# Performance work log

Hardware: AMD Instinct MI355X
Metric: run time of the kernel (lower is better)

The kernel has to match this reference:

```python
import jax, jax.numpy as jnp
import numpy as np

N, FIN, FOUT = 4096, 512, 256
ALPHA = 0.2          # LeakyReLU negative slope
NEG_INF = -9e15      # mask value from the torch source


def setup_inputs() -> dict:
    key = jax.random.key(0)
    ks = jax.random.split(key, 11)
    h = jax.random.normal(ks[0], (N, FIN), dtype=jnp.float32)
    adj_n = jax.random.randint(ks[1], (N, N), 0, 2, dtype=jnp.int32)
    adj_d = jax.random.randint(ks[2], (N, N), 0, 2, dtype=jnp.int32)
    G_nd = jax.random.normal(ks[3], (2, N, FOUT), dtype=jnp.float32)
    # learned parameters (xavier-ish scale)
    W_n = jax.random.normal(ks[4], (FIN, FOUT), dtype=jnp.float32) * 0.05
    a1_n = jax.random.normal(ks[5], (FOUT, 1), dtype=jnp.float32) * 0.05
    a2_n = jax.random.normal(ks[6], (FOUT, 1), dtype=jnp.float32) * 0.05
    W_d = jax.random.normal(ks[7], (FIN, FOUT), dtype=jnp.float32) * 0.05
    a1_d = jax.random.normal(ks[8], (FOUT, 1), dtype=jnp.float32) * 0.05
    a2_d = jax.random.normal(ks[9], (FOUT, 1), dtype=jnp.float32) * 0.05
    scale = jnp.zeros((1,), dtype=jnp.float32)
    return {"h": h, "adj_n": adj_n, "adj_d": adj_d, "G_nd": G_nd,
            "W_n": W_n, "a1_n": a1_n, "a2_n": a2_n,
            "W_d": W_d, "a1_d": a1_d, "a2_d": a2_d, "scale": scale}


def _gat(h, adj, W, a1, a2):
    # Wh: [N, FOUT]
    Wh = h @ W
    # outer-sum attention logits: e[i,j] = leakyrelu(Wh_i.a1 + Wh_j.a2)
    e = jax.nn.leaky_relu((Wh @ a1) + (Wh @ a2).T, negative_slope=ALPHA)  # [N, N]
    att = jnp.where(adj > 0, e, jnp.float32(NEG_INF))
    att = jax.nn.softmax(att, axis=-1)
    # dropout is identity in eval mode
    return jax.nn.elu(att @ Wh)  # [N, FOUT]


def reference(h, adj_n, adj_d, G_nd, W_n, a1_n, a2_n, W_d, a1_d, a2_d, scale):
    f_n_S = _gat(h, adj_n, W_n, a1_n, a2_n)
    f_d_S = _gat(h, adj_d, W_d, a1_d, a2_d)
    # The G_nd cross-attention branch (f_nd_C) in the torch source is computed
    # but never used in the returned value; omitted here (jit would DCE it).
    return f_n_S + f_d_S
```

## Files before the change

### kernel.cpp

```cpp
#include <hip/hip_runtime.h>

#define N_NODES 4096
#define FIN     512
#define FOUT    256
#define NSPLIT  4
#define NTILES  ((N_NODES / NSPLIT) / 64)

typedef __attribute__((ext_vector_type(8))) short bf16x8s;
typedef __attribute__((ext_vector_type(4))) float f32x4;
typedef __attribute__((ext_vector_type(8))) unsigned short u16x8;
typedef unsigned short u16;
typedef unsigned int   u32;
typedef unsigned long long u64;

__device__ inline u16 f2b(float f) {
    union { float f; unsigned int u; } v; v.f = f;
    unsigned int r = v.u + 0x7fffu + ((v.u >> 16) & 1u);
    return (u16)(r >> 16);
}

__global__ __launch_bounds__(256) void prep_kernel(
    const float* __restrict__ h, const float* __restrict__ Wn,
    const float* __restrict__ Wd,
    const int* __restrict__ adjn, const int* __restrict__ adjd,
    u16* __restrict__ hb, u16* __restrict__ WTb, u16* __restrict__ bits16,
    float* __restrict__ s12)
{
    __shared__ u16 tl[64 * 72];
    const int t = threadIdx.x;
    const int bid = blockIdx.x;

    if (bid < 1024) {
        int idx = (bid * 256 + t) * 8;
        float4 f0 = *(const float4*)&h[idx];
        float4 f1 = *(const float4*)&h[idx + 4];
        u16x8 o;
        o[0]=f2b(f0.x); o[1]=f2b(f0.y); o[2]=f2b(f0.z); o[3]=f2b(f0.w);
        o[4]=f2b(f1.x); o[5]=f2b(f1.y); o[6]=f2b(f1.z); o[7]=f2b(f1.w);
        *(u16x8*)&hb[idx] = o;
    } else if (bid < 3072) {
        const int lane = t & 63, w = t >> 6;
        const long gw = (long)(bid - 1024) * 4 + w;
        const long base = gw * 4096;
        const int* p = (base < (1L << 24)) ? (adjn + base)
                                           : (adjd + (base - (1L << 24)));
        const int4* src = (const int4*)p + lane * 4;
        u16* dst = bits16 + (base >> 4) + lane;
        #pragma unroll
        for (int s = 0; s < 4; ++s) {
            int4 a = src[s * 256 + 0];
            int4 b = src[s * 256 + 1];
            int4 c = src[s * 256 + 2];
            int4 d = src[s * 256 + 3];
            u32 m = 0;
            m |= (u32)(a.x > 0) << 0;  m |= (u32)(a.y > 0) << 1;
            m |= (u32)(a.z > 0) << 2;  m |= (u32)(a.w > 0) << 3;
            m |= (u32)(b.x > 0) << 4;  m |= (u32)(b.y > 0) << 5;
            m |= (u32)(b.z > 0) << 6;  m |= (u32)(b.w > 0) << 7;
            m |= (u32)(c.x > 0) << 8;  m |= (u32)(c.y > 0) << 9;
            m |= (u32)(c.z > 0) << 10; m |= (u32)(c.w > 0) << 11;
            m |= (u32)(d.x > 0) << 12; m |= (u32)(d.y > 0) << 13;
            m |= (u32)(d.z > 0) << 14; m |= (u32)(d.w > 0) << 15;
            dst[s * 64] = (u16)m;
        }
    } else if (bid < 3136) {
        int id = bid - 3072;
        int kx = id & 7, ny = (id >> 3) & 3, b = id >> 5;
        const float* W = b ? Wd : Wn;
        int k0 = kx * 64, n0 = ny * 64;
        int kr = t >> 2, nc0 = (t & 3) * 16;
        const float* src = W + (size_t)(k0 + kr) * FOUT + n0 + nc0;
        #pragma unroll
        for (int jv = 0; jv < 4; ++jv) {
            float4 f = *(const float4*)(src + jv * 4);
            tl[(nc0 + jv * 4 + 0) * 72 + kr] = f2b(f.x);
            tl[(nc0 + jv * 4 + 1) * 72 + kr] = f2b(f.y);
            tl[(nc0 + jv * 4 + 2) * 72 + kr] = f2b(f.z);
            tl[(nc0 + jv * 4 + 3) * 72 + kr] = f2b(f.w);
        }
        __syncthreads();
        int n = t >> 2, kc0 = (t & 3) * 16;
        u16* dst = WTb + ((size_t)b << 17) + (size_t)(n0 + n) * FIN + k0 + kc0;
        *(uint4*)dst       = *(uint4*)&tl[n * 72 + kc0];
        *(uint4*)(dst + 8) = *(uint4*)&tl[n * 72 + kc0 + 8];
    } else {
        float4 z = {0.f, 0.f, 0.f, 0.f};
        float4* p4 = (float4*)s12;
        #pragma unroll
        for (int k = 0; k < 16; ++k) p4[k * 256 + t] = z;
    }
}

__global__ __launch_bounds__(256) void wh_gemm_kernel(
    const u16* __restrict__ hb, const u16* __restrict__ WTb,
    const float* __restrict__ a1n, const float* __restrict__ a2n,
    const float* __restrict__ a1d, const float* __restrict__ a2d,
    u16* __restrict__ WhT, float* __restrict__ s1, float* __restrict__ s2)
{
    __shared__ u16 smem[8192];
    u16* a_lds = smem;
    u16* b_lds = smem + 4096;

    const int t = threadIdx.x, lane = t & 63, w = t >> 6;
    const int q = lane >> 4, ln = lane & 15;
    const int i0 = blockIdx.x * 64, n0 = blockIdx.y * 64, b = blockIdx.z;
    const u16* wt = WTb + ((size_t)b << 17);

    f32x4 acc[4];
    #pragma unroll
    for (int i = 0; i < 4; ++i) acc[i] = (f32x4){0.f, 0.f, 0.f, 0.f};

    for (int kt = 0; kt < 8; ++kt) {
        const int k0 = kt * 64;
        __syncthreads();
        #pragma unroll
        for (int it = 0; it < 2; ++it) {
            int chunk = it * 256 + t;
            int r = chunk >> 3, kc = chunk & 7;
            const u16* g = hb + (size_t)(i0 + r) * FIN + k0 + ((kc ^ (r & 7)) * 8);
            u16* l = a_lds + (it * 256 + w * 64) * 8;
            __builtin_amdgcn_global_load_lds(
                (const __attribute__((address_space(1))) void*)g,
                (__attribute__((address_space(3))) void*)l, 16, 0, 0);
        }
        #pragma unroll
        for (int it = 0; it < 2; ++it) {
            int chunk = it * 256 + t;
            int n = chunk >> 3, kc = chunk & 7;
            const u16* g = wt + (size_t)(n0 + n) * FIN + k0 + ((kc ^ (n & 7)) * 8);
            u16* l = b_lds + (it * 256 + w * 64) * 8;
            __builtin_amdgcn_global_load_lds(
                (const __attribute__((address_space(1))) void*)g,
                (__attribute__((address_space(3))) void*)l, 16, 0, 0);
        }
        __syncthreads();
        #pragma unroll
        for (int ks = 0; ks < 2; ++ks) {
            int sw = ((ks * 4 + q) ^ (ln & 7)) * 8;
            bf16x8s af = *(const bf16x8s*)&a_lds[(w * 16 + ln) * 64 + sw];
            #pragma unroll
            for (int nt = 0; nt < 4; ++nt) {
                bf16x8s bfv = *(const bf16x8s*)&b_lds[(nt * 16 + ln) * 64 + sw];
                acc[nt] = __builtin_amdgcn_mfma_f32_16x16x32_bf16(af, bfv, acc[nt], 0, 0, 0);
            }
        }
    }

    {
        const float* a1 = b ? a1d : a1n;
        const float* a2 = b ? a2d : a2n;
        float s1p[4] = {0.f, 0.f, 0.f, 0.f};
        float s2p[4] = {0.f, 0.f, 0.f, 0.f};
        #pragma unroll
        for (int nt = 0; nt < 4; ++nt) {
            float va1 = a1[n0 + nt * 16 + ln];
            float va2 = a2[n0 + nt * 16 + ln];
            #pragma unroll
            for (int r = 0; r < 4; ++r) {
                s1p[r] += acc[nt][r] * va1;
                s2p[r] += acc[nt][r] * va2;
            }
        }
        #pragma unroll
        for (int r = 0; r < 4; ++r) {
            #pragma unroll
            for (int off = 8; off >= 1; off >>= 1) {
                s1p[r] += __shfl_xor(s1p[r], off);
                s2p[r] += __shfl_xor(s2p[r], off);
            }
            if (ln == 0) {
                int row = i0 + w * 16 + q * 4 + r;
                atomicAdd(&s1[b * N_NODES + row], s1p[r]);
                atomicAdd(&s2[b * N_NODES + row], s2p[r]);
            }
        }
    }

    __syncthreads();
    #pragma unroll
    for (int nt = 0; nt < 4; ++nt)
        #pragma unroll
        for (int r = 0; r < 4; ++r)
            smem[(nt * 16 + ln) * 72 + (w * 16 + q * 4 + r)] = f2b(acc[nt][r]);
    __syncthreads();
    {
        const int nl = t >> 2, is = (t & 3) * 16;
        u16* dst = WhT + ((size_t)b << 20) + (size_t)(n0 + nl) * N_NODES + i0 + is;
        *(uint4*)dst       = *(uint4*)&smem[nl * 72 + is];
        *(uint4*)(dst + 8) = *(uint4*)&smem[nl * 72 + is + 8];
    }
}

__global__ __launch_bounds__(256) void attn_kernel(
    const u32* __restrict__ bits,
    const u16* __restrict__ WhT,
    const float* __restrict__ s1, const float* __restrict__ s2,
    float* __restrict__ num_ws, float* __restrict__ den_ws)
{
    __shared__ u16 wht_lds[256 * 64];
    __shared__ u16 p_lds[64 * 64];
    __shared__ float den_lds[64];

    const int t = threadIdx.x, lane = t & 63, w = t >> 6;
    const int q = lane >> 4, ln = lane & 15;
    const int b = blockIdx.z, split = blockIdx.y;
    const int i0 = blockIdx.x * 64;

    const u16* whtB = WhT + ((size_t)b << 20);
    const float* s1b = s1 + b * N_NODES;
    const float* s2b = s2 + b * N_NODES;

    const int pr = t >> 3;
    const int cw = t & 7;
    const int pc = cw * 8;
    const int bsh = (cw & 3) * 8;
    const float s1v0 = s1b[i0 + pr];
    const float s1v1 = s1b[i0 + pr + 32];
    const u32* bitrow0 = bits + (size_t)b * (N_NODES * (N_NODES / 32))
                              + (size_t)(i0 + pr) * (N_NODES / 32) + (cw >> 2);
    const u32* bitrow1 = bitrow0 + 32 * (N_NODES / 32);

    if (t < 64) den_lds[t] = 0.f;

    f32x4 acc[4][4];
    #pragma unroll
    for (int mt = 0; mt < 4; ++mt)
        #pragma unroll
        for (int nt = 0; nt < 4; ++nt) acc[mt][nt] = (f32x4){0.f, 0.f, 0.f, 0.f};

    const int jbase = split * (N_NODES / NSPLIT);
    u32 bw0_pf = bitrow0[jbase >> 5];
    u32 bw1_pf = bitrow1[jbase >> 5];
    float4 sv0_pf = *(const float4*)&s2b[jbase + pc];
    float4 sv1_pf = *(const float4*)&s2b[jbase + pc + 4];

    for (int jt = 0; jt < NTILES; ++jt) {
        const int j0 = jbase + jt * 64;
        __syncthreads();
        #pragma unroll
        for (int it = 0; it < 8; ++it) {
            int chunk = it * 256 + t;
            int n = chunk >> 3, kc = chunk & 7;
            const u16* g = whtB + (size_t)n * N_NODES + j0 + ((kc ^ (n & 7)) * 8);
            u16* l = wht_lds + (it * 256 + w * 64) * 8;
            __builtin_amdgcn_global_load_lds(
                (const __attribute__((address_space(1))) void*)g,
                (__attribute__((address_space(3))) void*)l, 16, 0, 0);
        }
        u32 bw0 = bw0_pf, bw1 = bw1_pf;
        float4 sv0 = sv0_pf, sv1 = sv1_pf;
        if (jt < NTILES - 1) {
            bw0_pf = bitrow0[(j0 + 64) >> 5];
            bw1_pf = bitrow1[(j0 + 64) >> 5];
            sv0_pf = *(const float4*)&s2b[j0 + 64 + pc];
            sv1_pf = *(const float4*)&s2b[j0 + 64 + pc + 4];
        }
        u32 m0 = (bw0 >> bsh) & 0xffu;
        u32 m1 = (bw1 >> bsh) & 0xffu;
        float svf[8] = {sv0.x, sv0.y, sv0.z, sv0.w, sv1.x, sv1.y, sv1.z, sv1.w};
        float d0 = 0.f, d1 = 0.f;
        u16x8 pk0, pk1;
        #pragma unroll
        for (int jj = 0; jj < 8; ++jj) {
            float sv = svf[jj];
            float x0 = s1v0 + sv, x1 = s1v1 + sv;
            float p0 = ((m0 >> jj) & 1u) ? __expf(fmaxf(x0, 0.2f * x0)) : 0.f;
            float p1 = ((m1 >> jj) & 1u) ? __expf(fmaxf(x1, 0.2f * x1)) : 0.f;
            d0 += p0; d1 += p1;
            pk0[jj] = f2b(p0); pk1[jj] = f2b(p1);
        }
        d0 += __shfl_down(d0, 4, 8); d1 += __shfl_down(d1, 4, 8);
        d0 += __shfl_down(d0, 2, 8); d1 += __shfl_down(d1, 2, 8);
        d0 += __shfl_down(d0, 1, 8); d1 += __shfl_down(d1, 1, 8);
        if ((t & 7) == 0) { den_lds[pr] += d0; den_lds[pr + 32] += d1; }
        int swp = ((cw ^ (pr & 7)) * 8);
        *(u16x8*)&p_lds[pr * 64 + swp] = pk0;
        *(u16x8*)&p_lds[(pr + 32) * 64 + swp] = pk1;
        __syncthreads();
        #pragma unroll
        for (int ks = 0; ks < 2; ++ks) {
            int sw = ((ks * 4 + q) ^ (ln & 7)) * 8;
            bf16x8s af[4];
            #pragma unroll
            for (int mt = 0; mt < 4; ++mt)
                af[mt] = *(const bf16x8s*)&p_lds[(mt * 16 + ln) * 64 + sw];
            #pragma unroll
            for (int nt = 0; nt < 4; ++nt) {
                bf16x8s bfv = *(const bf16x8s*)&wht_lds[(w * 64 + nt * 16 + ln) * 64 + sw];
                #pragma unroll
                for (int mt = 0; mt < 4; ++mt)
                    acc[mt][nt] = __builtin_amdgcn_mfma_f32_16x16x32_bf16(af[mt], bfv, acc[mt][nt], 0, 0, 0);
            }
        }
    }
    const size_t pbase = (size_t)(b * NSPLIT + split) * N_NODES;
    #pragma unroll
    for (int mt = 0; mt < 4; ++mt)
        #pragma unroll
        for (int r = 0; r < 4; ++r) {
            int row = mt * 16 + q * 4 + r;
            #pragma unroll
            for (int nt = 0; nt < 4; ++nt)
                num_ws[(pbase + i0 + row) * FOUT + w * 64 + nt * 16 + ln] = acc[mt][nt][r];
        }
    if (t < 64) den_ws[pbase + i0 + t] = den_lds[t];
}

__global__ __launch_bounds__(256) void reduce_kernel(
    const float* __restrict__ num_ws, const float* __restrict__ den_ws,
    float* __restrict__ out)
{
    int gid = blockIdx.x * 256 + threadIdx.x;
    int i = gid >> 6;
    int f4 = (gid & 63) * 4;
    float4 o = {0.f, 0.f, 0.f, 0.f};
    #pragma unroll
    for (int b = 0; b < 2; ++b) {
        float4 num = {0.f, 0.f, 0.f, 0.f};
        float den = 0.f;
        #pragma unroll
        for (int s = 0; s < NSPLIT; ++s) {
            const float4 v = *(const float4*)&num_ws[((size_t)(b * NSPLIT + s) * N_NODES + i) * FOUT + f4];
            num.x += v.x; num.y += v.y; num.z += v.z; num.w += v.w;
            den += den_ws[(size_t)(b * NSPLIT + s) * N_NODES + i];
        }
        float inv = 1.0f / den;
        float e0 = num.x * inv, e1 = num.y * inv, e2 = num.z * inv, e3 = num.w * inv;
        o.x += (e0 > 0.f) ? e0 : expm1f(e0);
        o.y += (e1 > 0.f) ? e1 : expm1f(e1);
        o.z += (e2 > 0.f) ? e2 : expm1f(e2);
        o.w += (e3 > 0.f) ? e3 : expm1f(e3);
    }
    *(float4*)&out[(size_t)i * FOUT + f4] = o;
}

extern "C" void kernel_launch(void* const* d_in, const int* in_sizes, int n_in,
                              void* d_out, int out_size, void* d_ws, size_t ws_size,
                              hipStream_t stream) {
    const float* h    = (const float*)d_in[0];
    const int*   adjn = (const int*)d_in[1];
    const int*   adjd = (const int*)d_in[2];
    const float* Wn   = (const float*)d_in[4];
    const float* a1n  = (const float*)d_in[5];
    const float* a2n  = (const float*)d_in[6];
    const float* Wd   = (const float*)d_in[7];
    const float* a1d  = (const float*)d_in[8];
    const float* a2d  = (const float*)d_in[9];

    char* ws = (char*)d_ws;
    u16*  WhT  = (u16*)ws;
    u16*  bits = (u16*)(ws + ((size_t)4 << 20));
    float* s1  = (float*)(ws + ((size_t)8 << 20));
    float* s2  = s1 + 2 * N_NODES;
    float* den = s2 + 2 * N_NODES;
    u16*  hb   = (u16*)(ws + ((size_t)8 << 20) + ((size_t)256 << 10));
    u16*  WTb  = (u16*)(ws + ((size_t)12 << 20) + ((size_t)256 << 10));
    float* num = (float*)(ws + ((size_t)8 << 20) + ((size_t)256 << 10));

    prep_kernel<<<3137, 256, 0, stream>>>(h, Wn, Wd, adjn, adjd, hb, WTb, bits, s1);
    wh_gemm_kernel<<<dim3(64, 4, 2), 256, 0, stream>>>(hb, WTb, a1n, a2n, a1d, a2d, WhT, s1, s2);
    attn_kernel<<<dim3(64, NSPLIT, 2), 256, 0, stream>>>((const u32*)bits, WhT, s1, s2, num, den);
    reduce_kernel<<<1024, 256, 0, stream>>>(num, den, (float*)d_out);
}
```

Baseline: 221.5 us.

## Read int adjacency directly in attention kernel instead of prepacking bitmasks

Removes the prep stage that packed both 4096x4096 int32 adjacency matrices into bitmasks, and has the attention kernel load int4 adjacency values directly with prefetch. This avoids one full read of the adjacency plus a bitmask write and reread across kernels. The attention kernel now streams 32x more mask bytes per tile (128 MB total), so it may become bandwidth-bound where it was not before.

```diff
diff --git a/kernel.cpp b/kernel.cpp
--- a/kernel.cpp
+++ b/kernel.cpp
@@ -11,7 +11,6 @@
 typedef __attribute__((ext_vector_type(8))) unsigned short u16x8;
 typedef unsigned short u16;
 typedef unsigned int   u32;
-typedef unsigned long long u64;
 
 __device__ inline u16 f2b(float f) {
     union { float f; unsigned int u; } v; v.f = f;
@@ -22,9 +21,7 @@
 __global__ __launch_bounds__(256) void prep_kernel(
     const float* __restrict__ h, const float* __restrict__ Wn,
     const float* __restrict__ Wd,
-    const int* __restrict__ adjn, const int* __restrict__ adjd,
-    u16* __restrict__ hb, u16* __restrict__ WTb, u16* __restrict__ bits16,
-    float* __restrict__ s12)
+    u16* __restrict__ hb, u16* __restrict__ WTb, float* __restrict__ s12)
 {
     __shared__ u16 tl[64 * 72];
     const int t = threadIdx.x;
@@ -38,33 +35,8 @@
         o[0]=f2b(f0.x); o[1]=f2b(f0.y); o[2]=f2b(f0.z); o[3]=f2b(f0.w);
         o[4]=f2b(f1.x); o[5]=f2b(f1.y); o[6]=f2b(f1.z); o[7]=f2b(f1.w);
         *(u16x8*)&hb[idx] = o;
-    } else if (bid < 3072) {
-        const int lane = t & 63, w = t >> 6;
-        const long gw = (long)(bid - 1024) * 4 + w;
-        const long base = gw * 4096;
-        const int* p = (base < (1L << 24)) ? (adjn + base)
-                                           : (adjd + (base - (1L << 24)));
-        const int4* src = (const int4*)p + lane * 4;
-        u16* dst = bits16 + (base >> 4) + lane;
-        #pragma unroll
-        for (int s = 0; s < 4; ++s) {
-            int4 a = src[s * 256 + 0];
-            int4 b = src[s * 256 + 1];
-            int4 c = src[s * 256 + 2];
-            int4 d = src[s * 256 + 3];
-            u32 m = 0;
-            m |= (u32)(a.x > 0) << 0;  m |= (u32)(a.y > 0) << 1;
-            m |= (u32)(a.z > 0) << 2;  m |= (u32)(a.w > 0) << 3;
-            m |= (u32)(b.x > 0) << 4;  m |= (u32)(b.y > 0) << 5;
-            m |= (u32)(b.z > 0) << 6;  m |= (u32)(b.w > 0) << 7;
-            m |= (u32)(c.x > 0) << 8;  m |= (u32)(c.y > 0) << 9;
-            m |= (u32)(c.z > 0) << 10; m |= (u32)(c.w > 0) << 11;
-            m |= (u32)(d.x > 0) << 12; m |= (u32)(d.y > 0) << 13;
-            m |= (u32)(d.z > 0) << 14; m |= (u32)(d.w > 0) << 15;
-            dst[s * 64] = (u16)m;
-        }
-    } else if (bid < 3136) {
-        int id = bid - 3072;
+    } else if (bid < 1088) {
+        int id = bid - 1024;
         int kx = id & 7, ny = (id >> 3) & 3, b = id >> 5;
         const float* W = b ? Wd : Wn;
         int k0 = kx * 64, n0 = ny * 64;
@@ -192,7 +164,7 @@
 }
 
 __global__ __launch_bounds__(256) void attn_kernel(
-    const u32* __restrict__ bits,
+    const int* __restrict__ adj_n, const int* __restrict__ adj_d,
     const u16* __restrict__ WhT,
     const float* __restrict__ s1, const float* __restrict__ s2,
     float* __restrict__ num_ws, float* __restrict__ den_ws)
@@ -206,6 +178,7 @@
     const int b = blockIdx.z, split = blockIdx.y;
     const int i0 = blockIdx.x * 64;
 
+    const int* adjb = b ? adj_d : adj_n;
     const u16* whtB = WhT + ((size_t)b << 20);
     const float* s1b = s1 + b * N_NODES;
     const float* s2b = s2 + b * N_NODES;
@@ -213,12 +186,10 @@
     const int pr = t >> 3;
     const int cw = t & 7;
     const int pc = cw * 8;
-    const int bsh = (cw & 3) * 8;
     const float s1v0 = s1b[i0 + pr];
     const float s1v1 = s1b[i0 + pr + 32];
-    const u32* bitrow0 = bits + (size_t)b * (N_NODES * (N_NODES / 32))
-                              + (size_t)(i0 + pr) * (N_NODES / 32) + (cw >> 2);
-    const u32* bitrow1 = bitrow0 + 32 * (N_NODES / 32);
+    const size_t arow0 = (size_t)(i0 + pr) * N_NODES + pc;
+    const size_t arow1 = arow0 + (size_t)32 * N_NODES;
 
     if (t < 64) den_lds[t] = 0.f;
 
@@ -229,8 +200,10 @@
         for (int nt = 0; nt < 4; ++nt) acc[mt][nt] = (f32x4){0.f, 0.f, 0.f, 0.f};
 
     const int jbase = split * (N_NODES / NSPLIT);
-    u32 bw0_pf = bitrow0[jbase >> 5];
-    u32 bw1_pf = bitrow1[jbase >> 5];
+    int4 a00_pf = *(const int4*)&adjb[arow0 + jbase];
+    int4 a01_pf = *(const int4*)&adjb[arow0 + jbase + 4];
+    int4 a10_pf = *(const int4*)&adjb[arow1 + jbase];
+    int4 a11_pf = *(const int4*)&adjb[arow1 + jbase + 4];
     float4 sv0_pf = *(const float4*)&s2b[jbase + pc];
     float4 sv1_pf = *(const float4*)&s2b[jbase + pc + 4];
 
@@ -247,16 +220,19 @@
                 (const __attribute__((address_space(1))) void*)g,
                 (__attribute__((address_space(3))) void*)l, 16, 0, 0);
         }
-        u32 bw0 = bw0_pf, bw1 = bw1_pf;
+        int4 a00 = a00_pf, a01 = a01_pf, a10 = a10_pf, a11 = a11_pf;
         float4 sv0 = sv0_pf, sv1 = sv1_pf;
         if (jt < NTILES - 1) {
-            bw0_pf = bitrow0[(j0 + 64) >> 5];
-            bw1_pf = bitrow1[(j0 + 64) >> 5];
-            sv0_pf = *(const float4*)&s2b[j0 + 64 + pc];
-            sv1_pf = *(const float4*)&s2b[j0 + 64 + pc + 4];
-        }
-        u32 m0 = (bw0 >> bsh) & 0xffu;
-        u32 m1 = (bw1 >> bsh) & 0xffu;
+            const int jn = j0 + 64;
+            a00_pf = *(const int4*)&adjb[arow0 + jn];
+            a01_pf = *(const int4*)&adjb[arow0 + jn + 4];
+            a10_pf = *(const int4*)&adjb[arow1 + jn];
+            a11_pf = *(const int4*)&adjb[arow1 + jn + 4];
+            sv0_pf = *(const float4*)&s2b[jn + pc];
+            sv1_pf = *(const float4*)&s2b[jn + pc + 4];
+        }
+        int v0[8] = {a00.x, a00.y, a00.z, a00.w, a01.x, a01.y, a01.z, a01.w};
+        int v1[8] = {a10.x, a10.y, a10.z, a10.w, a11.x, a11.y, a11.z, a11.w};
         float svf[8] = {sv0.x, sv0.y, sv0.z, sv0.w, sv1.x, sv1.y, sv1.z, sv1.w};
         float d0 = 0.f, d1 = 0.f;
         u16x8 pk0, pk1;
@@ -264,8 +240,8 @@
         for (int jj = 0; jj < 8; ++jj) {
             float sv = svf[jj];
             float x0 = s1v0 + sv, x1 = s1v1 + sv;
-            float p0 = ((m0 >> jj) & 1u) ? __expf(fmaxf(x0, 0.2f * x0)) : 0.f;
-            float p1 = ((m1 >> jj) & 1u) ? __expf(fmaxf(x1, 0.2f * x1)) : 0.f;
+            float p0 = (v0[jj] > 0) ? __expf(fmaxf(x0, 0.2f * x0)) : 0.f;
+            float p1 = (v1[jj] > 0) ? __expf(fmaxf(x1, 0.2f * x1)) : 0.f;
             d0 += p0; d1 += p1;
             pk0[jj] = f2b(p0); pk1[jj] = f2b(p1);
         }
@@ -349,7 +325,6 @@
 
     char* ws = (char*)d_ws;
     u16*  WhT  = (u16*)ws;
-    u16*  bits = (u16*)(ws + ((size_t)4 << 20));
     float* s1  = (float*)(ws + ((size_t)8 << 20));
     float* s2  = s1 + 2 * N_NODES;
     float* den = s2 + 2 * N_NODES;
@@ -357,8 +332,8 @@
     u16*  WTb  = (u16*)(ws + ((size_t)12 << 20) + ((size_t)256 << 10));
     float* num = (float*)(ws + ((size_t)8 << 20) + ((size_t)256 << 10));
 
-    prep_kernel<<<3137, 256, 0, stream>>>(h, Wn, Wd, adjn, adjd, hb, WTb, bits, s1);
+    prep_kernel<<<1089, 256, 0, stream>>>(h, Wn, Wd, hb, WTb, s1);
     wh_gemm_kernel<<<dim3(64, 4, 2), 256, 0, stream>>>(hb, WTb, a1n, a2n, a1d, a2d, WhT, s1, s2);
-    attn_kernel<<<dim3(64, NSPLIT, 2), 256, 0, stream>>>((const u32*)bits, WhT, s1, s2, num, den);
+    attn_kernel<<<dim3(64, NSPLIT, 2), 256, 0, stream>>>(adjn, adjd, WhT, s1, s2, num, den);
     reduce_kernel<<<1024, 256, 0, stream>>>(num, den, (float*)d_out);
 }
```

New measurement: 204.0 us. 1.09x faster.
